# Kernel optimization log

Measured on AMD Instinct MI355X. Metric: run time of the kernel, lower is better.

Reference implementation:

```python
import jax, jax.numpy as jnp
import numpy as np

N_NODES = 50000
N_EDGES = 800000
D_IN = 256
D_HID = 128


def setup_inputs() -> dict:
    key = jax.random.key(0)
    ks = jax.random.split(key, 10)
    x = jax.random.normal(ks[0], (N_NODES, D_IN), dtype=jnp.float32)
    edge_index = jax.random.randint(ks[1], (2, N_EDGES), 0, N_NODES, dtype=jnp.int64)
    # GCNConv params (glorot-ish init), 3 layers: 256->128, 128->128, 128->128
    def glorot(k, fan_in, fan_out):
        s = jnp.sqrt(6.0 / (fan_in + fan_out))
        return jax.random.uniform(k, (fan_in, fan_out), jnp.float32, -s, s)
    W0 = glorot(ks[2], D_IN, D_HID)
    b0 = jnp.zeros((D_HID,), jnp.float32)
    W1 = glorot(ks[3], D_HID, D_HID)
    b1 = jnp.zeros((D_HID,), jnp.float32)
    W2 = glorot(ks[4], D_HID, D_HID)
    b2 = jnp.zeros((D_HID,), jnp.float32)
    return {"x": x, "edge_index": edge_index, "W0": W0, "b0": b0,
            "W1": W1, "b1": b1, "W2": W2, "b2": b2}


def _gcn_conv(x, W, b, src, dst, deg_inv_sqrt, deg_inv):
    # PyG GCNConv: x' = D^{-1/2} (A + I) D^{-1/2} (x W) + b
    h = x @ W  # [N, d_out]
    norm = deg_inv_sqrt[src] * deg_inv_sqrt[dst]  # [E]
    msg = h[src] * norm[:, None]  # gather + scale, [E, d_out]
    agg = jax.ops.segment_sum(msg, dst, num_segments=x.shape[0])
    # self-loop contribution: norm = deg^{-1/2} * deg^{-1/2} = 1/deg
    return agg + h * deg_inv[:, None] + b


def reference(x, edge_index, W0, b0, W1, b1, W2, b2):
    src, dst = edge_index[0], edge_index[1]
    n = x.shape[0]
    # degree with self loops (computed on destination, source_to_target flow)
    deg = jax.ops.segment_sum(jnp.ones((src.shape[0],), x.dtype), dst,
                              num_segments=n) + 1.0
    deg_inv_sqrt = deg ** -0.5
    deg_inv = 1.0 / deg
    h = jax.nn.relu(_gcn_conv(x, W0, b0, src, dst, deg_inv_sqrt, deg_inv))
    h = jax.nn.relu(_gcn_conv(h, W1, b1, src, dst, deg_inv_sqrt, deg_inv))
    h = jax.nn.relu(_gcn_conv(h, W2, b2, src, dst, deg_inv_sqrt, deg_inv))
    return h
```

## Files before the change

### kernel.cpp

```cpp
#include <hip/hip_runtime.h>

#define N_NODES 50000
#define N_EDGES 800000
#define D_HID   128

typedef unsigned int uint;
typedef unsigned short ushort;
typedef __attribute__((ext_vector_type(8))) short short8;
typedef __attribute__((ext_vector_type(4))) float f32x4;

#define SCAN_NB ((N_NODES + 255) / 256)
#define NB       196
#define CAP      6144
#define P1_BLOCKS 200
#define P1_CHUNK  4000

__global__ __launch_bounds__(256) void part_k(const int* __restrict__ src,
                                              const int* __restrict__ dst,
                                              int* __restrict__ bcur,
                                              int2* __restrict__ ebuf, int e) {
    __shared__ int hist[NB];
    __shared__ int base[NB];
    int tid = threadIdx.x;
    if (tid < NB) hist[tid] = 0;
    __syncthreads();

    int e0 = blockIdx.x * P1_CHUNK;
    int2 ed[16];
    bool val[16];
#pragma unroll
    for (int i = 0; i < 16; ++i) {
        int o = i * 256 + tid;
        int idx = e0 + o;
        val[i] = (o < P1_CHUNK) && (idx < e);
        if (val[i]) {
            ed[i] = make_int2(src[idx], dst[idx]);
            atomicAdd(&hist[ed[i].y >> 8], 1);
        }
    }
    __syncthreads();
    if (tid < NB && hist[tid] > 0) base[tid] = atomicAdd(&bcur[tid], hist[tid]);
    __syncthreads();
    if (tid < NB) hist[tid] = 0;
    __syncthreads();
#pragma unroll
    for (int i = 0; i < 16; ++i) {
        if (val[i]) {
            int bk = ed[i].y >> 8;
            int o  = base[bk] + atomicAdd(&hist[bk], 1);
            if (o < CAP) ebuf[(size_t)bk * CAP + o] = ed[i];
        }
    }
}

__global__ __launch_bounds__(256) void bucket_cnt_k(const int2* __restrict__ ebuf,
                                                    const int* __restrict__ bcnt,
                                                    int* __restrict__ cnt, int n) {
    __shared__ int c[256];
    int b = blockIdx.x, tid = threadIdx.x;
    c[tid] = 0;
    __syncthreads();
    int m = bcnt[b]; if (m > CAP) m = CAP;
    for (int i = tid; i < m; i += 256)
        atomicAdd(&c[ebuf[(size_t)b * CAP + i].y & 255], 1);
    __syncthreads();
    int node = b * 256 + tid;
    if (node < n) cnt[node] = c[tid];
}

__global__ void bsum_k(const int* __restrict__ cnt, int* __restrict__ bsum, int n) {
    int i = blockIdx.x * 256 + threadIdx.x;
    int v = (i < n) ? cnt[i] : 0;
#pragma unroll
    for (int off = 32; off; off >>= 1) v += __shfl_down(v, off, 64);
    __shared__ int ws[4];
    int lane = threadIdx.x & 63, w = threadIdx.x >> 6;
    if (lane == 0) ws[w] = v;
    __syncthreads();
    if (threadIdx.x == 0) bsum[blockIdx.x] = ws[0] + ws[1] + ws[2] + ws[3];
}

__global__ void bscan_k(const int* __restrict__ bsum, int* __restrict__ boff,
                        int* __restrict__ row_ptr_end, int nb) {
    __shared__ int s[256];
    int t = threadIdx.x;
    int v = (t < nb) ? bsum[t] : 0;
    s[t] = v;
    __syncthreads();
    for (int off = 1; off < 256; off <<= 1) {
        int u = (t >= off) ? s[t - off] : 0;
        __syncthreads();
        s[t] += u;
        __syncthreads();
    }
    if (t < nb) boff[t] = s[t] - v;
    if (t == 255) *row_ptr_end = s[255];
}

__global__ void scan3_k(const int* __restrict__ cnt, const int* __restrict__ boff,
                        int* __restrict__ row_ptr, float* __restrict__ dis, int n) {
    __shared__ int s[256];
    int i = blockIdx.x * 256 + threadIdx.x;
    int t = threadIdx.x;
    int v = (i < n) ? cnt[i] : 0;
    s[t] = v;
    __syncthreads();
    for (int off = 1; off < 256; off <<= 1) {
        int u = (t >= off) ? s[t - off] : 0;
        __syncthreads();
        s[t] += u;
        __syncthreads();
    }
    if (i < n) {
        row_ptr[i] = boff[blockIdx.x] + s[t] - v;
        dis[i] = rsqrtf((float)v + 1.0f);
    }
}

__global__ __launch_bounds__(256) void csr_k(const int2* __restrict__ ebuf,
                                             const int* __restrict__ bcnt,
                                             const int* __restrict__ row_ptr,
                                             int* __restrict__ col, int n) {
    __shared__ int rp_l[257];
    __shared__ int cur[256];
    __shared__ int win[CAP];
    int b = blockIdx.x, tid = threadIdx.x;
    int node0 = b * 256;
    for (int i = tid; i < 257; i += 256) {
        int nd = node0 + i; if (nd > n) nd = n;
        rp_l[i] = row_ptr[nd];
    }
    cur[tid] = 0;
    __syncthreads();
    int base0 = rp_l[0];
    int m = bcnt[b]; if (m > CAP) m = CAP;

    for (int i = tid; i < m; i += 256) {
        int2 ed = ebuf[(size_t)b * CAP + i];
        int ll = ed.y & 255;
        int pos = rp_l[ll] + atomicAdd(&cur[ll], 1) - base0;
        win[pos] = ed.x;
    }
    __syncthreads();
    for (int i = tid; i < m; i += 256) col[base0 + i] = win[i];
}

__global__ __launch_bounds__(256) void rowsort_k(const int* __restrict__ rp,
                                                 int* __restrict__ col, int n) {
    int node = blockIdx.x * 4 + (threadIdx.x >> 6);
    if (node >= n) return;
    int lane = threadIdx.x & 63;
    int beg = rp[node], end = rp[node + 1];
    int len = end - beg;
    if (len <= 1) return;
    if (len <= 64) {
        int v = (lane < len) ? col[beg + lane] : 0x7fffffff;
#pragma unroll
        for (int k = 2; k <= 64; k <<= 1)
#pragma unroll
            for (int j = k >> 1; j > 0; j >>= 1) {
                int other = __shfl_xor(v, j);
                bool up    = (lane & k) == 0;
                bool small = (lane & j) == 0;
                v = (small == up) ? min(v, other) : max(v, other);
            }
        if (lane < len) col[beg + lane] = v;
    } else if (lane == 0) {
        for (int i = beg + 1; i < end; ++i) {
            int key = col[i]; int j = i - 1;
            while (j >= beg && col[j] > key) { col[j + 1] = col[j]; --j; }
            col[j + 1] = key;
        }
    }
}

__device__ inline ushort f2bf(float f) {
    unsigned u = __float_as_uint(f);
    unsigned rounding = 0x7fffu + ((u >> 16) & 1u);
    return (ushort)((u + rounding) >> 16);
}
__device__ inline float bf_lo(uint v) { return __uint_as_float(v << 16); }
__device__ inline float bf_hi(uint v) { return __uint_as_float(v & 0xffff0000u); }
__device__ inline short8 cvt8(float4 f0, float4 f1) {
    short8 r;
    r[0] = (short)f2bf(f0.x); r[1] = (short)f2bf(f0.y);
    r[2] = (short)f2bf(f0.z); r[3] = (short)f2bf(f0.w);
    r[4] = (short)f2bf(f1.x); r[5] = (short)f2bf(f1.y);
    r[6] = (short)f2bf(f1.z); r[7] = (short)f2bf(f1.w);
    return r;
}

__global__ void wtrans_all_k(const float* __restrict__ W0, const float* __restrict__ W1,
                             const float* __restrict__ W2, ushort* __restrict__ Wt0,
                             ushort* __restrict__ Wt1, ushort* __restrict__ Wt2,
                             uint* __restrict__ hb_padrow) {
    int i = blockIdx.x * 256 + threadIdx.x;
    if (i < 64) hb_padrow[i] = 0;
    const float* W; ushort* Wt; int K, j;
    if (i < 32768)      { W = W0; Wt = Wt0; K = 256; j = i; }
    else if (i < 49152) { W = W1; Wt = Wt1; K = 128; j = i - 32768; }
    else                { W = W2; Wt = Wt2; K = 128; j = i - 49152; }
    int k = j >> 7, n = j & 127;
    Wt[(size_t)n * K + k] = f2bf(W[j]);
}

template<int K, bool AF32>
__global__ __launch_bounds__(256, 3) void mfma_gemm_k(const void* __restrict__ Ap,
                                                      const ushort* __restrict__ Bt,
                                                      const float* __restrict__ dis,
                                                      ushort* __restrict__ H,
                                                      int M, int ntiles) {
    constexpr int T   = K / 32;
    constexpr int NC  = (K == 128) ? 4 : 2;
    constexpr int RPT = (K == 128) ? 32 : 16;
    int tid = threadIdx.x;
    int w = tid >> 6, l = tid & 63;
    int lr = l & 15, kg = (l >> 4) * 8;
    int rIn   = (K == 128) ? (w >> 1) * 16 : 0;
    int cBase = (K == 128) ? (w & 1) * 64 : w * 32;

    short8 b[NC][T];
#pragma unroll
    for (int c = 0; c < NC; ++c)
#pragma unroll
        for (int t = 0; t < T; ++t)
            b[c][t] = *(const short8*)&Bt[(size_t)(cBase + c * 16 + lr) * K + t * 32 + kg];

    int tile = blockIdx.x;
    if (tile >= ntiles) return;
    const int G = gridDim.x;

    auto loadA = [&](int tl, short8* dst) {
        int rc = tl * RPT + rIn + lr; if (rc >= M) rc = M - 1;
        if constexpr (AF32) {
            const float* A32 = (const float*)Ap;
#pragma unroll
            for (int t = 0; t < T; ++t) {
                float4 f0 = *(const float4*)&A32[(size_t)rc * K + t * 32 + kg];
                float4 f1 = *(const float4*)&A32[(size_t)rc * K + t * 32 + kg + 4];
                dst[t] = cvt8(f0, f1);
            }
        } else {
            const ushort* A16 = (const ushort*)Ap;
#pragma unroll
            for (int t = 0; t < T; ++t)
                dst[t] = *(const short8*)&A16[(size_t)rc * K + t * 32 + kg];
        }
    };

    short8 a[T];
    loadA(tile, a);
    for (; tile < ntiles; tile += G) {
        short8 an[T];
        int nt = tile + G;
        if (nt < ntiles) loadA(nt, an);

        f32x4 acc[NC];
#pragma unroll
        for (int c = 0; c < NC; ++c) acc[c] = (f32x4){0.f, 0.f, 0.f, 0.f};
#pragma unroll
        for (int t = 0; t < T; ++t)
#pragma unroll
            for (int c = 0; c < NC; ++c)
                acc[c] = __builtin_amdgcn_mfma_f32_16x16x32_bf16(a[t], b[c][t], acc[c], 0, 0, 0);

        int rs = tile * RPT + rIn + (l >> 4) * 4;
        float dsc[4];
#pragma unroll
        for (int j = 0; j < 4; ++j) dsc[j] = (rs + j < M) ? dis[rs + j] : 0.f;
#pragma unroll
        for (int c = 0; c < NC; ++c)
#pragma unroll
            for (int j = 0; j < 4; ++j) {
                int r = rs + j;
                if (r < M) H[(size_t)r * 128 + cBase + c * 16 + lr] = f2bf(acc[c][j] * dsc[j]);
            }
#pragma unroll
        for (int t = 0; t < T; ++t) a[t] = an[t];
    }
}

template<bool LAST>
__global__ __launch_bounds__(256) void aggregate_k(const ushort* __restrict__ hs,
                                                   const int* __restrict__ row_ptr,
                                                   const int* __restrict__ col,
                                                   const float* __restrict__ dis,
                                                   const float* __restrict__ bias,
                                                   ushort* __restrict__ act,
                                                   float* __restrict__ out, int n) {
    int node = blockIdx.x * 4 + (threadIdx.x >> 6);
    if (node >= n) return;
    int lane = threadIdx.x & 63;
    int g  = lane >> 4;
    int cl = lane & 15;
    const char* base = (const char*)hs + (cl << 4);

    float ax[8];
#pragma unroll
    for (int j = 0; j < 8; ++j) ax[j] = 0.f;

    int beg = row_ptr[node], end = row_ptr[node + 1];
    for (int e = beg; e < end; e += 32) {
        int s[8];
#pragma unroll
        for (int q = 0; q < 8; ++q) {
            int idx = e + q * 4 + g;
            s[q] = (idx < end) ? col[idx] : N_NODES;
        }
        uint4 u[8];
#pragma unroll
        for (int q = 0; q < 8; ++q)
            u[q] = *(const uint4*)(base + ((size_t)s[q] << 8));
#pragma unroll
        for (int q = 0; q < 8; ++q) {
            ax[0] += bf_lo(u[q].x); ax[1] += bf_hi(u[q].x);
            ax[2] += bf_lo(u[q].y); ax[3] += bf_hi(u[q].y);
            ax[4] += bf_lo(u[q].z); ax[5] += bf_hi(u[q].z);
            ax[6] += bf_lo(u[q].w); ax[7] += bf_hi(u[q].w);
        }
    }
#pragma unroll
    for (int j = 0; j < 8; ++j) {
        ax[j] += __shfl_xor(ax[j], 16);
        ax[j] += __shfl_xor(ax[j], 32);
    }
    if (g == 0) {
        float dn = dis[node];
        uint4 un = *(const uint4*)(base + ((size_t)node << 8));
        float hsn[8] = {bf_lo(un.x), bf_hi(un.x), bf_lo(un.y), bf_hi(un.y),
                        bf_lo(un.z), bf_hi(un.z), bf_lo(un.w), bf_hi(un.w)};
        int c0 = cl * 8;
        float4 bv0 = *(const float4*)&bias[c0];
        float4 bv1 = *(const float4*)&bias[c0 + 4];
        float bb[8] = {bv0.x, bv0.y, bv0.z, bv0.w, bv1.x, bv1.y, bv1.z, bv1.w};
        float o[8];
#pragma unroll
        for (int j = 0; j < 8; ++j)
            o[j] = fmaxf((ax[j] + hsn[j]) * dn + bb[j], 0.f);
        if (LAST) {
            *(float4*)&out[(size_t)node * D_HID + c0]     = make_float4(o[0], o[1], o[2], o[3]);
            *(float4*)&out[(size_t)node * D_HID + c0 + 4] = make_float4(o[4], o[5], o[6], o[7]);
        } else {
            uint4 p;
            p.x = (uint)f2bf(o[0]) | ((uint)f2bf(o[1]) << 16);
            p.y = (uint)f2bf(o[2]) | ((uint)f2bf(o[3]) << 16);
            p.z = (uint)f2bf(o[4]) | ((uint)f2bf(o[5]) << 16);
            p.w = (uint)f2bf(o[6]) | ((uint)f2bf(o[7]) << 16);
            *(uint4*)((char*)act + ((size_t)node << 8) + (cl << 4)) = p;
        }
    }
}

extern "C" void kernel_launch(void* const* d_in, const int* in_sizes, int n_in,
                              void* d_out, int out_size, void* d_ws, size_t ws_size,
                              hipStream_t stream) {
    const float* x  = (const float*)d_in[0];
    const int*   ei = (const int*)d_in[1];
    const float* W0 = (const float*)d_in[2];
    const float* b0 = (const float*)d_in[3];
    const float* W1 = (const float*)d_in[4];
    const float* b1 = (const float*)d_in[5];
    const float* W2 = (const float*)d_in[6];
    const float* b2 = (const float*)d_in[7];
    float* out = (float*)d_out;

    const int N = N_NODES, E = N_EDGES;
    const int* src = ei;
    const int* dst = ei + E;

    char* w = (char*)d_ws;
    size_t off = 0;
    auto alloc = [&](size_t bytes) {
        size_t o = off;
        off += (bytes + 255) & ~(size_t)255;
        return o;
    };
    int*    cnt    = (int*)(w + alloc((size_t)N * 4));
    int*    bcur   = (int*)(w + alloc((size_t)NB * 4));
    float*  dis    = (float*)(w + alloc((size_t)N * 4));
    int*    rp     = (int*)(w + alloc((size_t)(N + 1) * 4));
    int*    bsum   = (int*)(w + alloc((size_t)SCAN_NB * 4));
    int*    boff   = (int*)(w + alloc((size_t)SCAN_NB * 4));
    int*    col    = (int*)(w + alloc((size_t)E * 4));
    int2*   ebuf   = (int2*)(w + alloc((size_t)NB * CAP * 8));
    ushort* hb     = (ushort*)(w + alloc((size_t)(N + 1) * D_HID * 2));
    ushort* act    = (ushort*)(w + alloc((size_t)N * D_HID * 2));
    ushort* Wt0    = (ushort*)(w + alloc((size_t)128 * 256 * 2));
    ushort* Wt1    = (ushort*)(w + alloc((size_t)128 * 128 * 2));
    ushort* Wt2    = (ushort*)(w + alloc((size_t)128 * 128 * 2));
    (void)ws_size; (void)n_in; (void)in_sizes; (void)out_size;

    hipMemsetAsync(bcur, 0, (size_t)NB * 4, stream);

    part_k<<<P1_BLOCKS, 256, 0, stream>>>(src, dst, bcur, ebuf, E);
    bucket_cnt_k<<<NB, 256, 0, stream>>>(ebuf, bcur, cnt, N);
    bsum_k<<<SCAN_NB, 256, 0, stream>>>(cnt, bsum, N);
    bscan_k<<<1, 256, 0, stream>>>(bsum, boff, rp + N, SCAN_NB);
    scan3_k<<<SCAN_NB, 256, 0, stream>>>(cnt, boff, rp, dis, N);
    csr_k<<<NB, 256, 0, stream>>>(ebuf, bcur, rp, col, N);
    rowsort_k<<<(N + 3) / 4, 256, 0, stream>>>(rp, col, N);

    wtrans_all_k<<<256, 256, 0, stream>>>(W0, W1, W2, Wt0, Wt1, Wt2,
                                          (uint*)(hb + (size_t)N * D_HID));

    const int GG = 768;
    int nt256 = (N + 15) / 16;
    int nt128 = (N + 31) / 32;
    int agg_grid = (N + 3) / 4;

    mfma_gemm_k<256, true><<<GG, 256, 0, stream>>>(x, Wt0, dis, hb, N, nt256);
    aggregate_k<false><<<agg_grid, 256, 0, stream>>>(hb, rp, col, dis, b0, act, out, N);
    mfma_gemm_k<128, false><<<GG, 256, 0, stream>>>(act, Wt1, dis, hb, N, nt128);
    aggregate_k<false><<<agg_grid, 256, 0, stream>>>(hb, rp, col, dis, b1, act, out, N);
    mfma_gemm_k<128, false><<<GG, 256, 0, stream>>>(act, Wt2, dis, hb, N, nt128);
    aggregate_k<true><<<agg_grid, 256, 0, stream>>>(hb, rp, col, dis, b2, act, out, N);
}
```

Baseline: 260.2 us.

## Stage A tiles in swizzled LDS with one 64-row tile per block

Replaces the persistent register-prefetch GEMM with a kernel where each block loads a 64-row A tile into LDS with coalesced 16-byte loads and an XOR swizzle, then each wave computes 64 rows by 32 columns with MFMA. This is meant to improve global load coalescing and reuse the B fragments held in registers across four row blocks. In exchange the grid becomes one block per tile with no software prefetch across tiles, and the fp32 layer-0 tile uses 64KB of LDS per block, which limits occupancy.

```diff
diff --git a/kernel.cpp b/kernel.cpp
--- a/kernel.cpp
+++ b/kernel.cpp
@@ -205,78 +205,84 @@
 }
 
 template<int K, bool AF32>
-__global__ __launch_bounds__(256, 3) void mfma_gemm_k(const void* __restrict__ Ap,
-                                                      const ushort* __restrict__ Bt,
-                                                      const float* __restrict__ dis,
-                                                      ushort* __restrict__ H,
-                                                      int M, int ntiles) {
-    constexpr int T   = K / 32;
-    constexpr int NC  = (K == 128) ? 4 : 2;
-    constexpr int RPT = (K == 128) ? 32 : 16;
+__global__ __launch_bounds__(256) void gemm_lds_k(const void* __restrict__ Ap,
+                                                  const ushort* __restrict__ Bt,
+                                                  const float* __restrict__ dis,
+                                                  ushort* __restrict__ H,
+                                                  int M) {
+    constexpr int T  = K / 32;
+    constexpr int EB = AF32 ? 4 : 2;
+    constexpr int RS = K * EB;
+    constexpr int NL = (64 * RS) / 4096;
+    __shared__ char As[64 * RS];
+
     int tid = threadIdx.x;
-    int w = tid >> 6, l = tid & 63;
-    int lr = l & 15, kg = (l >> 4) * 8;
-    int rIn   = (K == 128) ? (w >> 1) * 16 : 0;
-    int cBase = (K == 128) ? (w & 1) * 64 : w * 32;
-
-    short8 b[NC][T];
-#pragma unroll
-    for (int c = 0; c < NC; ++c)
+    int w = tid >> 6, l = tid & 63, lr = l & 15, hi = l >> 4;
+    int cBase = w * 32;
+
+    short8 b[2][T];
+#pragma unroll
+    for (int c = 0; c < 2; ++c)
 #pragma unroll
         for (int t = 0; t < T; ++t)
-            b[c][t] = *(const short8*)&Bt[(size_t)(cBase + c * 16 + lr) * K + t * 32 + kg];
-
-    int tile = blockIdx.x;
-    if (tile >= ntiles) return;
-    const int G = gridDim.x;
-
-    auto loadA = [&](int tl, short8* dst) {
-        int rc = tl * RPT + rIn + lr; if (rc >= M) rc = M - 1;
-        if constexpr (AF32) {
-            const float* A32 = (const float*)Ap;
-#pragma unroll
-            for (int t = 0; t < T; ++t) {
-                float4 f0 = *(const float4*)&A32[(size_t)rc * K + t * 32 + kg];
-                float4 f1 = *(const float4*)&A32[(size_t)rc * K + t * 32 + kg + 4];
-                dst[t] = cvt8(f0, f1);
+            b[c][t] = *(const short8*)&Bt[(size_t)(cBase + c * 16 + lr) * K + t * 32 + hi * 8];
+
+    int r0 = blockIdx.x * 64;
+    const char* gbase = (const char*)Ap + (size_t)r0 * RS;
+
+#pragma unroll
+    for (int i = 0; i < NL; ++i) {
+        int L   = i * 4096 + tid * 16;
+        int row = L / RS;
+        int cb  = (L % RS) >> 4;
+        const char* srcp = (r0 + row < M) ? (gbase + (size_t)row * RS + ((size_t)cb << 4))
+                                          : gbase;
+        uint4 v = *(const uint4*)srcp;
+        *(uint4*)&As[row * RS + ((cb ^ (row & 7)) << 4)] = v;
+    }
+    __syncthreads();
+
+    f32x4 acc[4][2];
+#pragma unroll
+    for (int rb = 0; rb < 4; ++rb)
+#pragma unroll
+        for (int c = 0; c < 2; ++c) acc[rb][c] = (f32x4){0.f, 0.f, 0.f, 0.f};
+
+#pragma unroll
+    for (int rb = 0; rb < 4; ++rb) {
+        int row = rb * 16 + lr;
+        int s = row & 7;
+        const char* rbase = &As[row * RS];
+#pragma unroll
+        for (int t = 0; t < T; ++t) {
+            short8 a;
+            if constexpr (AF32) {
+                int cb0 = t * 8 + hi * 2;
+                float4 f0 = *(const float4*)(rbase + ((cb0 ^ s) << 4));
+                float4 f1 = *(const float4*)(rbase + (((cb0 + 1) ^ s) << 4));
+                a = cvt8(f0, f1);
+            } else {
+                int cb0 = t * 4 + hi;
+                a = *(const short8*)(rbase + ((cb0 ^ s) << 4));
             }
-        } else {
-            const ushort* A16 = (const ushort*)Ap;
-#pragma unroll
-            for (int t = 0; t < T; ++t)
-                dst[t] = *(const short8*)&A16[(size_t)rc * K + t * 32 + kg];
-        }
-    };
-
-    short8 a[T];
-    loadA(tile, a);
-    for (; tile < ntiles; tile += G) {
-        short8 an[T];
-        int nt = tile + G;
-        if (nt < ntiles) loadA(nt, an);
-
-        f32x4 acc[NC];
-#pragma unroll
-        for (int c = 0; c < NC; ++c) acc[c] = (f32x4){0.f, 0.f, 0.f, 0.f};
-#pragma unroll
-        for (int t = 0; t < T; ++t)
-#pragma unroll
-            for (int c = 0; c < NC; ++c)
-                acc[c] = __builtin_amdgcn_mfma_f32_16x16x32_bf16(a[t], b[c][t], acc[c], 0, 0, 0);
-
-        int rs = tile * RPT + rIn + (l >> 4) * 4;
-        float dsc[4];
-#pragma unroll
-        for (int j = 0; j < 4; ++j) dsc[j] = (rs + j < M) ? dis[rs + j] : 0.f;
-#pragma unroll
-        for (int c = 0; c < NC; ++c)
-#pragma unroll
-            for (int j = 0; j < 4; ++j) {
-                int r = rs + j;
-                if (r < M) H[(size_t)r * 128 + cBase + c * 16 + lr] = f2bf(acc[c][j] * dsc[j]);
+#pragma unroll
+            for (int c = 0; c < 2; ++c)
+                acc[rb][c] = __builtin_amdgcn_mfma_f32_16x16x32_bf16(a, b[c][t], acc[rb][c], 0, 0, 0);
+        }
+    }
+
+#pragma unroll
+    for (int rb = 0; rb < 4; ++rb) {
+#pragma unroll
+        for (int j = 0; j < 4; ++j) {
+            int r = r0 + rb * 16 + hi * 4 + j;
+            if (r < M) {
+                float d = dis[r];
+#pragma unroll
+                for (int c = 0; c < 2; ++c)
+                    H[(size_t)r * 128 + cBase + c * 16 + lr] = f2bf(acc[rb][c][j] * d);
             }
-#pragma unroll
-        for (int t = 0; t < T; ++t) a[t] = an[t];
+        }
     }
 }
 
@@ -403,15 +409,13 @@
     wtrans_all_k<<<256, 256, 0, stream>>>(W0, W1, W2, Wt0, Wt1, Wt2,
                                           (uint*)(hb + (size_t)N * D_HID));
 
-    const int GG = 768;
-    int nt256 = (N + 15) / 16;
-    int nt128 = (N + 31) / 32;
+    int nt64 = (N + 63) / 64;
     int agg_grid = (N + 3) / 4;
 
-    mfma_gemm_k<256, true><<<GG, 256, 0, stream>>>(x, Wt0, dis, hb, N, nt256);
+    gemm_lds_k<256, true><<<nt64, 256, 0, stream>>>(x, Wt0, dis, hb, N);
     aggregate_k<false><<<agg_grid, 256, 0, stream>>>(hb, rp, col, dis, b0, act, out, N);
-    mfma_gemm_k<128, false><<<GG, 256, 0, stream>>>(act, Wt1, dis, hb, N, nt128);
+    gemm_lds_k<128, false><<<nt64, 256, 0, stream>>>(act, Wt1, dis, hb, N);
     aggregate_k<false><<<agg_grid, 256, 0, stream>>>(hb, rp, col, dis, b1, act, out, N);
-    mfma_gemm_k<128, false><<<GG, 256, 0, stream>>>(act, Wt2, dis, hb, N, nt128);
+    gemm_lds_k<128, false><<<nt64, 256, 0, stream>>>(act, Wt2, dis, hb, N);
     aggregate_k<true><<<agg_grid, 256, 0, stream>>>(hb, rp, col, dis, b2, act, out, N);
 }
```

Result: faster. 232.3 us (-10.7%).
